# Kernel tuning notes

Measured on AMD Instinct MI355X. Metric: run time of the kernel, lower is better.

## Reference

```python
import jax, jax.numpy as jnp
import numpy as np

N = 50000   # nodes
E = 600000  # edges
F = 128     # feat_in
H = 64      # hidden_features
H2 = 32     # hidden_features // 2


def setup_inputs() -> dict:
    key = jax.random.key(0)
    ks = jax.random.split(key, 10)
    w = lambda k, shape: jax.random.normal(k, shape, dtype=jnp.float32) * 0.05
    return {
        "x": jax.random.normal(ks[0], (N, F), dtype=jnp.float32),
        "edge_index": jax.random.randint(ks[1], (2, E), 0, N, dtype=jnp.int32),
        "edge_attr": jax.random.uniform(ks[2], (E, 1), dtype=jnp.float32),
        # GINConv 1 MLP: Linear(F,H) -> Linear(H,H), learnable eps
        "w1a": w(ks[3], (H, F)), "b1a": jnp.zeros((H,), jnp.float32),
        "w1b": w(ks[4], (H, H)), "b1b": jnp.zeros((H,), jnp.float32),
        "eps1": jnp.zeros((), jnp.float32),
        # GINConv 2 MLP: Linear(H,H2) -> Linear(H2,H2), learnable eps
        "w2a": w(ks[5], (H2, H)), "b2a": jnp.zeros((H2,), jnp.float32),
        "w2b": w(ks[6], (H2, H2)), "b2b": jnp.zeros((H2,), jnp.float32),
        "eps2": jnp.zeros((), jnp.float32),
        # SAGEConv(H2, 1): lin_l (neighbor path, has bias), lin_r (root path, no bias)
        "wl": w(ks[7], (1, H2)), "bl": jnp.zeros((1,), jnp.float32),
        "wr": w(ks[8], (1, H2)),
    }


def _gin(x, src, dst, eps, wa, ba, wb, bb):
    # GIN: MLP((1+eps)*x_i + sum_{j->i} x_j)
    agg = jax.ops.segment_sum(x[src], dst, num_segments=x.shape[0])
    h = (1.0 + eps) * x + agg
    h = h @ wa.T + ba
    return h @ wb.T + bb


def reference(x, edge_index, edge_attr, w1a, b1a, w1b, b1b, eps1,
              w2a, b2a, w2b, b2b, eps2, wl, bl, wr):
    src, dst = edge_index[0], edge_index[1]
    ew = edge_attr.squeeze()  # (E,)
    n = x.shape[0]

    h = jax.nn.relu(_gin(x, src, dst, eps1, w1a, b1a, w1b, b1b))
    # dropout is identity in eval mode
    h = jax.nn.relu(_gin(h, src, dst, eps2, w2a, b2a, w2b, b2b))

    # SAGEConv with edge weights: mean over weighted messages + root transform
    msg = ew[:, None] * h[src]                                   # (E, H2)
    num = jax.ops.segment_sum(msg, dst, num_segments=n)          # (N, H2)
    cnt = jax.ops.segment_sum(jnp.ones((msg.shape[0],), h.dtype), dst, num_segments=n)
    mean = num / jnp.maximum(cnt, 1.0)[:, None]
    out = mean @ wl.T + bl + h @ wr.T                            # (N, 1)
    return jax.nn.relu(out)
```

## Files before the change

### kernel.cpp

```cpp
#include <hip/hip_runtime.h>

#define N_NODES 50000
#define N_EDGES 600000
#define F_IN 128
#define H1 64
#define H2 32
#define NBLK ((N_NODES + 255) / 256)
#define PREP_BLOCKS 41
#define CNT_BLOCKS ((N_EDGES / 4 + 255) / 256)
#define GEMM1_BLOCKS ((N_NODES + 63) / 64)
#define FILL_BLOCKS ((N_EDGES / 4 + 255) / 256)

__device__ inline unsigned bf_round(float x) {
  unsigned u = __float_as_uint(x);
  u += 0x7FFFu + ((u >> 16) & 1u);
  return u >> 16;
}
__device__ inline unsigned pack_bf2(float a, float b) {
  return (bf_round(b) << 16) | bf_round(a);
}
__device__ inline float2 unpack_bf2(unsigned u) {
  return make_float2(__uint_as_float(u << 16), __uint_as_float(u & 0xFFFF0000u));
}

__global__ __launch_bounds__(256) void prep_and_count(
    const float* __restrict__ w1a, const float* __restrict__ b1a,
    const float* __restrict__ w1b, const float* __restrict__ b1b,
    const float* __restrict__ w2a, const float* __restrict__ b2a,
    const float* __restrict__ w2b, const float* __restrict__ b2b,
    float* __restrict__ M1, float* __restrict__ c1,
    float* __restrict__ M2, float* __restrict__ c2,
    const int* __restrict__ ei, int* __restrict__ counts) {
  if (blockIdx.x >= PREP_BLOCKS) {
    int t = (blockIdx.x - PREP_BLOCKS) * 256 + threadIdx.x;
    if (t < N_EDGES / 4) {
      int4 d4 = *reinterpret_cast<const int4*>(&ei[N_EDGES + t * 4]);
      atomicAdd(&counts[d4.x], 1);
      atomicAdd(&counts[d4.y], 1);
      atomicAdd(&counts[d4.z], 1);
      atomicAdd(&counts[d4.w], 1);
    }
    return;
  }
  int i = blockIdx.x * 256 + threadIdx.x;
  if (i < F_IN * H1) {
    int f = i >> 6, h = i & 63;
    float s = 0.f;
    for (int m = 0; m < H1; ++m) s += w1a[m * F_IN + f] * w1b[h * H1 + m];
    M1[i] = s;
    return;
  }
  i -= F_IN * H1;
  if (i < H1) {
    float s = b1b[i];
    for (int m = 0; m < H1; ++m) s += b1a[m] * w1b[i * H1 + m];
    c1[i] = s;
    return;
  }
  i -= H1;
  if (i < H1 * H2) {
    int h = i >> 5, o = i & 31;
    float s = 0.f;
    for (int m = 0; m < H2; ++m) s += w2a[m * H1 + h] * w2b[o * H2 + m];
    M2[i] = s;
    return;
  }
  i -= H1 * H2;
  if (i < H2) {
    float s = b2b[i];
    for (int m = 0; m < H2; ++m) s += b2a[m] * w2b[i * H2 + m];
    c2[i] = s;
  }
}

__global__ __launch_bounds__(256) void block_sums(const int* __restrict__ counts,
                                                  int* __restrict__ bsums) {
  __shared__ int s[256];
  int t = threadIdx.x;
  int i = blockIdx.x * 256 + t;
  s[t] = (i < N_NODES) ? counts[i] : 0;
  __syncthreads();
  for (int off = 128; off > 0; off >>= 1) {
    if (t < off) s[t] += s[t + off];
    __syncthreads();
  }
  if (t == 0) bsums[blockIdx.x] = s[0];
}

__global__ __launch_bounds__(256) void emit_rowptr(const int* __restrict__ counts,
                                                   const int* __restrict__ bsums,
                                                   int* __restrict__ row_ptr,
                                                   int* __restrict__ cursor) {
  __shared__ int sb[256];
  __shared__ int s[256];
  int t = threadIdx.x;
  int bv = (t < NBLK) ? bsums[t] : 0;
  sb[t] = bv;
  __syncthreads();
  for (int off = 1; off < 256; off <<= 1) {
    int u = (t >= off) ? sb[t - off] : 0;
    __syncthreads();
    sb[t] += u;
    __syncthreads();
  }
  if (blockIdx.x == 0 && t == NBLK - 1) row_ptr[N_NODES] = sb[t];
  int boff = (blockIdx.x == 0) ? 0 : sb[blockIdx.x - 1];
  int i = blockIdx.x * 256 + t;
  int v = (i < N_NODES) ? counts[i] : 0;
  s[t] = v;
  __syncthreads();
  for (int off = 1; off < 256; off <<= 1) {
    int u = (t >= off) ? s[t - off] : 0;
    __syncthreads();
    s[t] += u;
    __syncthreads();
  }
  if (i < N_NODES) {
    int ex = boff + s[t] - v;
    row_ptr[i] = ex;
    cursor[i] = ex;
  }
}

__global__ __launch_bounds__(256) void gemm1_fill(
    const float* __restrict__ x, const float* __restrict__ M1,
    unsigned* __restrict__ ybf, const int* __restrict__ ei,
    const float* __restrict__ ea, int* __restrict__ cursor,
    int2* __restrict__ csr) {
  __shared__ float sW[F_IN * H1];
  __shared__ float sX[32][H1];
  if (blockIdx.x >= GEMM1_BLOCKS) {
    int t = (blockIdx.x - GEMM1_BLOCKS) * 256 + threadIdx.x;
    if (t < N_EDGES / 4) {
      int4 s4 = *reinterpret_cast<const int4*>(&ei[4 * t]);
      int4 d4 = *reinterpret_cast<const int4*>(&ei[N_EDGES + 4 * t]);
      float4 w4 = *reinterpret_cast<const float4*>(&ea[4 * t]);
      int p0 = atomicAdd(&cursor[d4.x], 1);
      csr[p0] = make_int2(s4.x, __float_as_int(w4.x));
      int p1 = atomicAdd(&cursor[d4.y], 1);
      csr[p1] = make_int2(s4.y, __float_as_int(w4.y));
      int p2 = atomicAdd(&cursor[d4.z], 1);
      csr[p2] = make_int2(s4.z, __float_as_int(w4.z));
      int p3 = atomicAdd(&cursor[d4.w], 1);
      csr[p3] = make_int2(s4.w, __float_as_int(w4.w));
    }
    return;
  }
  int tid = threadIdx.x;
  for (int i = tid; i < F_IN * H1; i += 256) sW[i] = M1[i];

  int row0 = blockIdx.x * 64;
  int tr = tid >> 4;
  int tc = tid & 15;
  int lrow = tid & 63;
  int kgrp = tid >> 6;
  const float* xrow = x + (long long)(row0 + lrow) * F_IN;
  bool rvalid = (row0 + lrow) < N_NODES;

  float acc[4][4] = {{0.f}};

  for (int kc = 0; kc < 4; ++kc) {
    float4 v0 = make_float4(0.f, 0.f, 0.f, 0.f);
    float4 v1 = make_float4(0.f, 0.f, 0.f, 0.f);
    if (rvalid) {
      v0 = *reinterpret_cast<const float4*>(xrow + kc * 32 + kgrp * 8);
      v1 = *reinterpret_cast<const float4*>(xrow + kc * 32 + kgrp * 8 + 4);
    }
    __syncthreads();
    sX[kgrp * 8 + 0][lrow] = v0.x;
    sX[kgrp * 8 + 1][lrow] = v0.y;
    sX[kgrp * 8 + 2][lrow] = v0.z;
    sX[kgrp * 8 + 3][lrow] = v0.w;
    sX[kgrp * 8 + 4][lrow] = v1.x;
    sX[kgrp * 8 + 5][lrow] = v1.y;
    sX[kgrp * 8 + 6][lrow] = v1.z;
    sX[kgrp * 8 + 7][lrow] = v1.w;
    __syncthreads();
#pragma unroll
    for (int k = 0; k < 32; ++k) {
      float4 a = *reinterpret_cast<const float4*>(&sX[k][tr * 4]);
      float4 b = *reinterpret_cast<const float4*>(&sW[(kc * 32 + k) * H1 + tc * 4]);
      acc[0][0] += a.x * b.x; acc[0][1] += a.x * b.y;
      acc[0][2] += a.x * b.z; acc[0][3] += a.x * b.w;
      acc[1][0] += a.y * b.x; acc[1][1] += a.y * b.y;
      acc[1][2] += a.y * b.z; acc[1][3] += a.y * b.w;
      acc[2][0] += a.z * b.x; acc[2][1] += a.z * b.y;
      acc[2][2] += a.z * b.z; acc[2][3] += a.z * b.w;
      acc[3][0] += a.w * b.x; acc[3][1] += a.w * b.y;
      acc[3][2] += a.w * b.z; acc[3][3] += a.w * b.w;
    }
  }
#pragma unroll
  for (int i = 0; i < 4; ++i) {
    int row = row0 + tr * 4 + i;
    if (row < N_NODES) {
      uint2 o;
      o.x = pack_bf2(acc[i][0], acc[i][1]);
      o.y = pack_bf2(acc[i][2], acc[i][3]);
      *reinterpret_cast<uint2*>(&ybf[(unsigned)row * 32 + tc * 2]) = o;
    }
  }
}

__global__ __launch_bounds__(256) void agg_h(
    const unsigned* __restrict__ ybf, const int* __restrict__ row_ptr,
    const int2* __restrict__ csr, const float* __restrict__ c1,
    const float* __restrict__ eps1p, float* __restrict__ h) {
  int tid = threadIdx.x;
  int node = blockIdx.x * 4 + (tid >> 6);
  if (node >= N_NODES) return;
  int lane = tid & 63;
  int half = lane >> 5;
  int j = lane & 31;
  int start = row_ptr[node], end = row_ptr[node + 1];
  int mid = start + ((end - start + 1) >> 1);
  int b0 = half ? mid : start;
  int b1 = half ? end : mid;
  float a0 = 0.f, a1 = 0.f;
  int e = b0;
  for (; e + 4 <= b1; e += 4) {
    int s0 = csr[e + 0].x;
    int s1 = csr[e + 1].x;
    int s2 = csr[e + 2].x;
    int s3 = csr[e + 3].x;
    float2 u0 = unpack_bf2(ybf[(unsigned)s0 * 32 + j]);
    float2 u1 = unpack_bf2(ybf[(unsigned)s1 * 32 + j]);
    float2 u2 = unpack_bf2(ybf[(unsigned)s2 * 32 + j]);
    float2 u3 = unpack_bf2(ybf[(unsigned)s3 * 32 + j]);
    a0 += (u0.x + u1.x) + (u2.x + u3.x);
    a1 += (u0.y + u1.y) + (u2.y + u3.y);
  }
  float2 t0 = make_float2(0.f, 0.f), t1 = make_float2(0.f, 0.f),
         t2 = make_float2(0.f, 0.f);
  if (e + 0 < b1) t0 = unpack_bf2(ybf[(unsigned)csr[e + 0].x * 32 + j]);
  if (e + 1 < b1) t1 = unpack_bf2(ybf[(unsigned)csr[e + 1].x * 32 + j]);
  if (e + 2 < b1) t2 = unpack_bf2(ybf[(unsigned)csr[e + 2].x * 32 + j]);
  a0 += (t0.x + t1.x) + t2.x;
  a1 += (t0.y + t1.y) + t2.y;
  a0 += __shfl_xor(a0, 32);
  a1 += __shfl_xor(a1, 32);
  if (half == 0) {
    float eps1 = 1.0f + *eps1p;
    float2 self = unpack_bf2(ybf[(unsigned)node * 32 + j]);
    float2 c = *reinterpret_cast<const float2*>(&c1[2 * j]);
    float2 hv;
    hv.x = fmaxf(eps1 * self.x + a0 + c.x, 0.f);
    hv.y = fmaxf(eps1 * self.y + a1 + c.y, 0.f);
    *reinterpret_cast<float2*>(&h[(unsigned)node * H1 + 2 * j]) = hv;
  }
}

__global__ __launch_bounds__(256) void gemm2(const float* __restrict__ h,
                                             const float* __restrict__ M2,
                                             unsigned* __restrict__ zbf) {
  __shared__ float sW[H1 * H2];
  __shared__ float sX[H1][64];
  int tid = threadIdx.x;
  for (int i = tid; i < H1 * H2; i += 256) sW[i] = M2[i];

  int row0 = blockIdx.x * 64;
  int lrow = tid & 63;
  int kg = tid >> 6;
  bool rv = (row0 + lrow) < N_NODES;
  float4 v[4] = {};
  if (rv) {
    const float* hr = h + (long long)(row0 + lrow) * H1 + kg * 16;
#pragma unroll
    for (int q = 0; q < 4; ++q) v[q] = *reinterpret_cast<const float4*>(hr + q * 4);
  }
#pragma unroll
  for (int q = 0; q < 4; ++q) {
    sX[kg * 16 + q * 4 + 0][lrow] = v[q].x;
    sX[kg * 16 + q * 4 + 1][lrow] = v[q].y;
    sX[kg * 16 + q * 4 + 2][lrow] = v[q].z;
    sX[kg * 16 + q * 4 + 3][lrow] = v[q].w;
  }
  __syncthreads();
  int tr = tid >> 4;
  int tc = tid & 15;
  float acc[4][2] = {{0.f}};
#pragma unroll
  for (int k = 0; k < H1; ++k) {
    float4 a = *reinterpret_cast<const float4*>(&sX[k][tr * 4]);
    float2 b = *reinterpret_cast<const float2*>(&sW[k * H2 + tc * 2]);
    acc[0][0] += a.x * b.x; acc[0][1] += a.x * b.y;
    acc[1][0] += a.y * b.x; acc[1][1] += a.y * b.y;
    acc[2][0] += a.z * b.x; acc[2][1] += a.z * b.y;
    acc[3][0] += a.w * b.x; acc[3][1] += a.w * b.y;
  }
#pragma unroll
  for (int i = 0; i < 4; ++i) {
    int row = row0 + tr * 4 + i;
    if (row < N_NODES)
      zbf[(unsigned)row * 16 + tc] = pack_bf2(acc[i][0], acc[i][1]);
  }
}

__global__ __launch_bounds__(256) void gin3(
    const unsigned* __restrict__ zbf, const int* __restrict__ row_ptr,
    const int2* __restrict__ csr, const float* __restrict__ c2,
    const float* __restrict__ eps2p, const float* __restrict__ wl,
    const float* __restrict__ wr, float* __restrict__ p,
    float* __restrict__ r) {
  int tid = blockIdx.x * 256 + threadIdx.x;
  int node = tid >> 4;
  if (node >= N_NODES) return;
  int j = tid & 15;
  int start = row_ptr[node], end = row_ptr[node + 1];
  float a0 = 0.f, a1 = 0.f;
  int e = start;
  for (; e + 8 <= end; e += 8) {
    int s0 = csr[e + 0].x; int s1 = csr[e + 1].x;
    int s2 = csr[e + 2].x; int s3 = csr[e + 3].x;
    int s4 = csr[e + 4].x; int s5 = csr[e + 5].x;
    int s6 = csr[e + 6].x; int s7 = csr[e + 7].x;
    float2 u0 = unpack_bf2(zbf[(unsigned)s0 * 16 + j]);
    float2 u1 = unpack_bf2(zbf[(unsigned)s1 * 16 + j]);
    float2 u2 = unpack_bf2(zbf[(unsigned)s2 * 16 + j]);
    float2 u3 = unpack_bf2(zbf[(unsigned)s3 * 16 + j]);
    float2 u4 = unpack_bf2(zbf[(unsigned)s4 * 16 + j]);
    float2 u5 = unpack_bf2(zbf[(unsigned)s5 * 16 + j]);
    float2 u6 = unpack_bf2(zbf[(unsigned)s6 * 16 + j]);
    float2 u7 = unpack_bf2(zbf[(unsigned)s7 * 16 + j]);
    a0 += ((u0.x + u1.x) + (u2.x + u3.x)) + ((u4.x + u5.x) + (u6.x + u7.x));
    a1 += ((u0.y + u1.y) + (u2.y + u3.y)) + ((u4.y + u5.y) + (u6.y + u7.y));
  }
  for (; e + 4 <= end; e += 4) {
    int s0 = csr[e + 0].x; int s1 = csr[e + 1].x;
    int s2 = csr[e + 2].x; int s3 = csr[e + 3].x;
    float2 u0 = unpack_bf2(zbf[(unsigned)s0 * 16 + j]);
    float2 u1 = unpack_bf2(zbf[(unsigned)s1 * 16 + j]);
    float2 u2 = unpack_bf2(zbf[(unsigned)s2 * 16 + j]);
    float2 u3 = unpack_bf2(zbf[(unsigned)s3 * 16 + j]);
    a0 += (u0.x + u1.x) + (u2.x + u3.x);
    a1 += (u0.y + u1.y) + (u2.y + u3.y);
  }
  float2 t0 = make_float2(0.f, 0.f), t1 = make_float2(0.f, 0.f),
         t2 = make_float2(0.f, 0.f);
  if (e + 0 < end) t0 = unpack_bf2(zbf[(unsigned)csr[e + 0].x * 16 + j]);
  if (e + 1 < end) t1 = unpack_bf2(zbf[(unsigned)csr[e + 1].x * 16 + j]);
  if (e + 2 < end) t2 = unpack_bf2(zbf[(unsigned)csr[e + 2].x * 16 + j]);
  a0 += (t0.x + t1.x) + t2.x;
  a1 += (t0.y + t1.y) + t2.y;
  float eps2 = 1.0f + *eps2p;
  float2 self = unpack_bf2(zbf[(unsigned)node * 16 + j]);
  float2 c = *reinterpret_cast<const float2*>(&c2[2 * j]);
  float h0 = fmaxf(eps2 * self.x + a0 + c.x, 0.f);
  float h1 = fmaxf(eps2 * self.y + a1 + c.y, 0.f);
  float2 l = *reinterpret_cast<const float2*>(&wl[2 * j]);
  float2 w = *reinterpret_cast<const float2*>(&wr[2 * j]);
  float pd = h0 * l.x + h1 * l.y;
  float rd = h0 * w.x + h1 * w.y;
#pragma unroll
  for (int m = 8; m >= 1; m >>= 1) {
    pd += __shfl_xor(pd, m, 16);
    rd += __shfl_xor(rd, m, 16);
  }
  if (j == 0) {
    p[node] = pd;
    r[node] = rd;
  }
}

__global__ __launch_bounds__(256) void sage_out(
    const int* __restrict__ row_ptr, const int2* __restrict__ csr,
    const float* __restrict__ p, const float* __restrict__ r,
    const float* __restrict__ blp, float* __restrict__ out) {
  int idx = blockIdx.x * 256 + threadIdx.x;
  int node = idx >> 4;
  if (node >= N_NODES) return;
  int l = idx & 15;
  int start = row_ptr[node], end = row_ptr[node + 1];
  float acc = 0.f;
  for (int e = start + l; e < end; e += 16) {
    int2 c = csr[e];
    acc += __int_as_float(c.y) * p[c.x];
  }
#pragma unroll
  for (int m = 8; m >= 1; m >>= 1) acc += __shfl_xor(acc, m, 16);
  if (l == 0) {
    float mean = acc / fmaxf((float)(end - start), 1.0f);
    out[node] = fmaxf(mean + blp[0] + r[node], 0.f);
  }
}

extern "C" void kernel_launch(void* const* d_in, const int* in_sizes, int n_in,
                              void* d_out, int out_size, void* d_ws,
                              size_t ws_size, hipStream_t stream) {
  const float* x = (const float*)d_in[0];
  const int* ei = (const int*)d_in[1];
  const float* ea = (const float*)d_in[2];
  const float* w1a = (const float*)d_in[3];
  const float* b1a = (const float*)d_in[4];
  const float* w1b = (const float*)d_in[5];
  const float* b1b = (const float*)d_in[6];
  const float* eps1 = (const float*)d_in[7];
  const float* w2a = (const float*)d_in[8];
  const float* b2a = (const float*)d_in[9];
  const float* w2b = (const float*)d_in[10];
  const float* b2b = (const float*)d_in[11];
  const float* eps2 = (const float*)d_in[12];
  const float* wl = (const float*)d_in[13];
  const float* bl = (const float*)d_in[14];
  const float* wr = (const float*)d_in[15];
  float* out = (float*)d_out;

  float* ws = (float*)d_ws;
  float* M1 = ws;
  float* c1 = M1 + F_IN * H1;
  float* M2 = c1 + H1;
  float* c2 = M2 + H1 * H2;
  unsigned* ybf = (unsigned*)(c2 + H2);
  float* h = (float*)(ybf + (size_t)N_NODES * 32);
  unsigned* zbf = (unsigned*)(h + (size_t)N_NODES * H1);
  float* p = (float*)(zbf + (size_t)N_NODES * 16);
  float* r = p + N_NODES;
  int2* csr = (int2*)(r + N_NODES);
  int* counts = (int*)(csr + N_EDGES);
  int* cursor = counts + N_NODES;
  int* bsums = cursor + N_NODES;
  int* row_ptr = bsums + NBLK;

  hipMemsetAsync(counts, 0, sizeof(int) * (size_t)N_NODES, stream);

  prep_and_count<<<PREP_BLOCKS + CNT_BLOCKS, 256, 0, stream>>>(
      w1a, b1a, w1b, b1b, w2a, b2a, w2b, b2b, M1, c1, M2, c2, ei, counts);

  block_sums<<<NBLK, 256, 0, stream>>>(counts, bsums);
  emit_rowptr<<<NBLK, 256, 0, stream>>>(counts, bsums, row_ptr, cursor);

  gemm1_fill<<<GEMM1_BLOCKS + FILL_BLOCKS, 256, 0, stream>>>(
      x, M1, ybf, ei, ea, cursor, csr);

  agg_h<<<(N_NODES + 3) / 4, 256, 0, stream>>>(ybf, row_ptr, csr, c1, eps1, h);

  gemm2<<<(N_NODES + 63) / 64, 256, 0, stream>>>(h, M2, zbf);

  gin3<<<(N_NODES * 16 + 255) / 256, 256, 0, stream>>>(zbf, row_ptr, csr, c2,
                                                       eps2, wl, wr, p, r);

  sage_out<<<(N_NODES * 16 + 255) / 256, 256, 0, stream>>>(row_ptr, csr, p, r,
                                                           bl, out);
}
```

Measured before the change: 223.0 us.

## Replace two-pass scan with atomic segment allocation and widen gather loads

Merges the block-sum and row-pointer scan kernels into one kernel that reserves each block's CSR range with an atomicAdd on a global counter. Segments are no longer in node order, so each node's end now comes from the cursor left by the fill pass instead of row_ptr[node+1]. The two gather kernels are also reorganized: each lane loads 8 bytes (four bf16 values) and several edges are gathered in parallel within a wavefront, then reduced with shuffles. The change removes one launch and one scan pass and aims for more memory parallelism in the gathers, at the cost of a non-deterministic CSR ordering and extra shuffle reductions.

```diff
diff --git a/kernel.cpp b/kernel.cpp
--- a/kernel.cpp
+++ b/kernel.cpp
@@ -73,38 +73,12 @@
   }
 }
 
-__global__ __launch_bounds__(256) void block_sums(const int* __restrict__ counts,
-                                                  int* __restrict__ bsums) {
+__global__ __launch_bounds__(256) void assign_segments(
+    const int* __restrict__ counts, int* __restrict__ total,
+    int* __restrict__ row_ptr, int* __restrict__ cursor) {
   __shared__ int s[256];
+  __shared__ int base;
   int t = threadIdx.x;
-  int i = blockIdx.x * 256 + t;
-  s[t] = (i < N_NODES) ? counts[i] : 0;
-  __syncthreads();
-  for (int off = 128; off > 0; off >>= 1) {
-    if (t < off) s[t] += s[t + off];
-    __syncthreads();
-  }
-  if (t == 0) bsums[blockIdx.x] = s[0];
-}
-
-__global__ __launch_bounds__(256) void emit_rowptr(const int* __restrict__ counts,
-                                                   const int* __restrict__ bsums,
-                                                   int* __restrict__ row_ptr,
-                                                   int* __restrict__ cursor) {
-  __shared__ int sb[256];
-  __shared__ int s[256];
-  int t = threadIdx.x;
-  int bv = (t < NBLK) ? bsums[t] : 0;
-  sb[t] = bv;
-  __syncthreads();
-  for (int off = 1; off < 256; off <<= 1) {
-    int u = (t >= off) ? sb[t - off] : 0;
-    __syncthreads();
-    sb[t] += u;
-    __syncthreads();
-  }
-  if (blockIdx.x == 0 && t == NBLK - 1) row_ptr[N_NODES] = sb[t];
-  int boff = (blockIdx.x == 0) ? 0 : sb[blockIdx.x - 1];
   int i = blockIdx.x * 256 + t;
   int v = (i < N_NODES) ? counts[i] : 0;
   s[t] = v;
@@ -115,8 +89,10 @@
     s[t] += u;
     __syncthreads();
   }
+  if (t == 255) base = atomicAdd(total, s[255]);
+  __syncthreads();
   if (i < N_NODES) {
-    int ex = boff + s[t] - v;
+    int ex = base + s[t] - v;
     row_ptr[i] = ex;
     cursor[i] = ex;
   }
@@ -204,49 +180,56 @@
 
 __global__ __launch_bounds__(256) void agg_h(
     const unsigned* __restrict__ ybf, const int* __restrict__ row_ptr,
-    const int2* __restrict__ csr, const float* __restrict__ c1,
-    const float* __restrict__ eps1p, float* __restrict__ h) {
+    const int* __restrict__ row_end, const int2* __restrict__ csr,
+    const float* __restrict__ c1, const float* __restrict__ eps1p,
+    float* __restrict__ h) {
   int tid = threadIdx.x;
   int node = blockIdx.x * 4 + (tid >> 6);
   if (node >= N_NODES) return;
   int lane = tid & 63;
-  int half = lane >> 5;
-  int j = lane & 31;
-  int start = row_ptr[node], end = row_ptr[node + 1];
-  int mid = start + ((end - start + 1) >> 1);
-  int b0 = half ? mid : start;
-  int b1 = half ? end : mid;
-  float a0 = 0.f, a1 = 0.f;
-  int e = b0;
-  for (; e + 4 <= b1; e += 4) {
-    int s0 = csr[e + 0].x;
-    int s1 = csr[e + 1].x;
-    int s2 = csr[e + 2].x;
-    int s3 = csr[e + 3].x;
-    float2 u0 = unpack_bf2(ybf[(unsigned)s0 * 32 + j]);
-    float2 u1 = unpack_bf2(ybf[(unsigned)s1 * 32 + j]);
-    float2 u2 = unpack_bf2(ybf[(unsigned)s2 * 32 + j]);
-    float2 u3 = unpack_bf2(ybf[(unsigned)s3 * 32 + j]);
-    a0 += (u0.x + u1.x) + (u2.x + u3.x);
-    a1 += (u0.y + u1.y) + (u2.y + u3.y);
-  }
-  float2 t0 = make_float2(0.f, 0.f), t1 = make_float2(0.f, 0.f),
-         t2 = make_float2(0.f, 0.f);
-  if (e + 0 < b1) t0 = unpack_bf2(ybf[(unsigned)csr[e + 0].x * 32 + j]);
-  if (e + 1 < b1) t1 = unpack_bf2(ybf[(unsigned)csr[e + 1].x * 32 + j]);
-  if (e + 2 < b1) t2 = unpack_bf2(ybf[(unsigned)csr[e + 2].x * 32 + j]);
-  a0 += (t0.x + t1.x) + t2.x;
-  a1 += (t0.y + t1.y) + t2.y;
-  a0 += __shfl_xor(a0, 32);
-  a1 += __shfl_xor(a1, 32);
-  if (half == 0) {
+  int g = lane >> 4;
+  int q = lane & 15;
+  int start = row_ptr[node], end = row_end[node];
+  float a0 = 0.f, a1 = 0.f, a2 = 0.f, a3 = 0.f;
+  for (int e0 = start; e0 < end; e0 += 16) {
+    int e_0 = e0 + g;
+    int e_1 = e0 + 4 + g;
+    int e_2 = e0 + 8 + g;
+    int e_3 = e0 + 12 + g;
+    uint2 v0 = make_uint2(0u, 0u), v1 = make_uint2(0u, 0u),
+          v2 = make_uint2(0u, 0u), v3 = make_uint2(0u, 0u);
+    if (e_0 < end)
+      v0 = *reinterpret_cast<const uint2*>(&ybf[(unsigned)csr[e_0].x * 32 + q * 2]);
+    if (e_1 < end)
+      v1 = *reinterpret_cast<const uint2*>(&ybf[(unsigned)csr[e_1].x * 32 + q * 2]);
+    if (e_2 < end)
+      v2 = *reinterpret_cast<const uint2*>(&ybf[(unsigned)csr[e_2].x * 32 + q * 2]);
+    if (e_3 < end)
+      v3 = *reinterpret_cast<const uint2*>(&ybf[(unsigned)csr[e_3].x * 32 + q * 2]);
+    float2 u00 = unpack_bf2(v0.x), u01 = unpack_bf2(v0.y);
+    float2 u10 = unpack_bf2(v1.x), u11 = unpack_bf2(v1.y);
+    float2 u20 = unpack_bf2(v2.x), u21 = unpack_bf2(v2.y);
+    float2 u30 = unpack_bf2(v3.x), u31 = unpack_bf2(v3.y);
+    a0 += (u00.x + u10.x) + (u20.x + u30.x);
+    a1 += (u00.y + u10.y) + (u20.y + u30.y);
+    a2 += (u01.x + u11.x) + (u21.x + u31.x);
+    a3 += (u01.y + u11.y) + (u21.y + u31.y);
+  }
+  a0 += __shfl_xor(a0, 16); a0 += __shfl_xor(a0, 32);
+  a1 += __shfl_xor(a1, 16); a1 += __shfl_xor(a1, 32);
+  a2 += __shfl_xor(a2, 16); a2 += __shfl_xor(a2, 32);
+  a3 += __shfl_xor(a3, 16); a3 += __shfl_xor(a3, 32);
+  if (g == 0) {
     float eps1 = 1.0f + *eps1p;
-    float2 self = unpack_bf2(ybf[(unsigned)node * 32 + j]);
-    float2 c = *reinterpret_cast<const float2*>(&c1[2 * j]);
-    float2 hv;
-    hv.x = fmaxf(eps1 * self.x + a0 + c.x, 0.f);
-    hv.y = fmaxf(eps1 * self.y + a1 + c.y, 0.f);
-    *reinterpret_cast<float2*>(&h[(unsigned)node * H1 + 2 * j]) = hv;
+    uint2 sv = *reinterpret_cast<const uint2*>(&ybf[(unsigned)node * 32 + q * 2]);
+    float2 s0 = unpack_bf2(sv.x), s1 = unpack_bf2(sv.y);
+    float4 c = *reinterpret_cast<const float4*>(&c1[4 * q]);
+    float4 hv;
+    hv.x = fmaxf(eps1 * s0.x + a0 + c.x, 0.f);
+    hv.y = fmaxf(eps1 * s0.y + a1 + c.y, 0.f);
+    hv.z = fmaxf(eps1 * s1.x + a2 + c.z, 0.f);
+    hv.w = fmaxf(eps1 * s1.y + a3 + c.w, 0.f);
+    *reinterpret_cast<float4*>(&h[(unsigned)node * H1 + 4 * q]) = hv;
   }
 }
 
@@ -298,79 +281,78 @@
 
 __global__ __launch_bounds__(256) void gin3(
     const unsigned* __restrict__ zbf, const int* __restrict__ row_ptr,
-    const int2* __restrict__ csr, const float* __restrict__ c2,
-    const float* __restrict__ eps2p, const float* __restrict__ wl,
-    const float* __restrict__ wr, float* __restrict__ p,
-    float* __restrict__ r) {
-  int tid = blockIdx.x * 256 + threadIdx.x;
-  int node = tid >> 4;
+    const int* __restrict__ row_end, const int2* __restrict__ csr,
+    const float* __restrict__ c2, const float* __restrict__ eps2p,
+    const float* __restrict__ wl, const float* __restrict__ wr,
+    float* __restrict__ p, float* __restrict__ r) {
+  int idx = blockIdx.x * 256 + threadIdx.x;
+  int node = idx >> 5;
   if (node >= N_NODES) return;
-  int j = tid & 15;
-  int start = row_ptr[node], end = row_ptr[node + 1];
-  float a0 = 0.f, a1 = 0.f;
-  int e = start;
-  for (; e + 8 <= end; e += 8) {
-    int s0 = csr[e + 0].x; int s1 = csr[e + 1].x;
-    int s2 = csr[e + 2].x; int s3 = csr[e + 3].x;
-    int s4 = csr[e + 4].x; int s5 = csr[e + 5].x;
-    int s6 = csr[e + 6].x; int s7 = csr[e + 7].x;
-    float2 u0 = unpack_bf2(zbf[(unsigned)s0 * 16 + j]);
-    float2 u1 = unpack_bf2(zbf[(unsigned)s1 * 16 + j]);
-    float2 u2 = unpack_bf2(zbf[(unsigned)s2 * 16 + j]);
-    float2 u3 = unpack_bf2(zbf[(unsigned)s3 * 16 + j]);
-    float2 u4 = unpack_bf2(zbf[(unsigned)s4 * 16 + j]);
-    float2 u5 = unpack_bf2(zbf[(unsigned)s5 * 16 + j]);
-    float2 u6 = unpack_bf2(zbf[(unsigned)s6 * 16 + j]);
-    float2 u7 = unpack_bf2(zbf[(unsigned)s7 * 16 + j]);
-    a0 += ((u0.x + u1.x) + (u2.x + u3.x)) + ((u4.x + u5.x) + (u6.x + u7.x));
-    a1 += ((u0.y + u1.y) + (u2.y + u3.y)) + ((u4.y + u5.y) + (u6.y + u7.y));
-  }
-  for (; e + 4 <= end; e += 4) {
-    int s0 = csr[e + 0].x; int s1 = csr[e + 1].x;
-    int s2 = csr[e + 2].x; int s3 = csr[e + 3].x;
-    float2 u0 = unpack_bf2(zbf[(unsigned)s0 * 16 + j]);
-    float2 u1 = unpack_bf2(zbf[(unsigned)s1 * 16 + j]);
-    float2 u2 = unpack_bf2(zbf[(unsigned)s2 * 16 + j]);
-    float2 u3 = unpack_bf2(zbf[(unsigned)s3 * 16 + j]);
-    a0 += (u0.x + u1.x) + (u2.x + u3.x);
-    a1 += (u0.y + u1.y) + (u2.y + u3.y);
-  }
-  float2 t0 = make_float2(0.f, 0.f), t1 = make_float2(0.f, 0.f),
-         t2 = make_float2(0.f, 0.f);
-  if (e + 0 < end) t0 = unpack_bf2(zbf[(unsigned)csr[e + 0].x * 16 + j]);
-  if (e + 1 < end) t1 = unpack_bf2(zbf[(unsigned)csr[e + 1].x * 16 + j]);
-  if (e + 2 < end) t2 = unpack_bf2(zbf[(unsigned)csr[e + 2].x * 16 + j]);
-  a0 += (t0.x + t1.x) + t2.x;
-  a1 += (t0.y + t1.y) + t2.y;
-  float eps2 = 1.0f + *eps2p;
-  float2 self = unpack_bf2(zbf[(unsigned)node * 16 + j]);
-  float2 c = *reinterpret_cast<const float2*>(&c2[2 * j]);
-  float h0 = fmaxf(eps2 * self.x + a0 + c.x, 0.f);
-  float h1 = fmaxf(eps2 * self.y + a1 + c.y, 0.f);
-  float2 l = *reinterpret_cast<const float2*>(&wl[2 * j]);
-  float2 w = *reinterpret_cast<const float2*>(&wr[2 * j]);
-  float pd = h0 * l.x + h1 * l.y;
-  float rd = h0 * w.x + h1 * w.y;
-#pragma unroll
-  for (int m = 8; m >= 1; m >>= 1) {
-    pd += __shfl_xor(pd, m, 16);
-    rd += __shfl_xor(rd, m, 16);
-  }
-  if (j == 0) {
-    p[node] = pd;
-    r[node] = rd;
+  int l = idx & 31;
+  int g = l >> 3;
+  int q = l & 7;
+  int start = row_ptr[node], end = row_end[node];
+  float a0 = 0.f, a1 = 0.f, a2 = 0.f, a3 = 0.f;
+  for (int e0 = start; e0 < end; e0 += 16) {
+    int e_0 = e0 + g;
+    int e_1 = e0 + 4 + g;
+    int e_2 = e0 + 8 + g;
+    int e_3 = e0 + 12 + g;
+    uint2 v0 = make_uint2(0u, 0u), v1 = make_uint2(0u, 0u),
+          v2 = make_uint2(0u, 0u), v3 = make_uint2(0u, 0u);
+    if (e_0 < end)
+      v0 = *reinterpret_cast<const uint2*>(&zbf[(unsigned)csr[e_0].x * 16 + q * 2]);
+    if (e_1 < end)
+      v1 = *reinterpret_cast<const uint2*>(&zbf[(unsigned)csr[e_1].x * 16 + q * 2]);
+    if (e_2 < end)
+      v2 = *reinterpret_cast<const uint2*>(&zbf[(unsigned)csr[e_2].x * 16 + q * 2]);
+    if (e_3 < end)
+      v3 = *reinterpret_cast<const uint2*>(&zbf[(unsigned)csr[e_3].x * 16 + q * 2]);
+    float2 u00 = unpack_bf2(v0.x), u01 = unpack_bf2(v0.y);
+    float2 u10 = unpack_bf2(v1.x), u11 = unpack_bf2(v1.y);
+    float2 u20 = unpack_bf2(v2.x), u21 = unpack_bf2(v2.y);
+    float2 u30 = unpack_bf2(v3.x), u31 = unpack_bf2(v3.y);
+    a0 += (u00.x + u10.x) + (u20.x + u30.x);
+    a1 += (u00.y + u10.y) + (u20.y + u30.y);
+    a2 += (u01.x + u11.x) + (u21.x + u31.x);
+    a3 += (u01.y + u11.y) + (u21.y + u31.y);
+  }
+  a0 += __shfl_xor(a0, 8, 32); a0 += __shfl_xor(a0, 16, 32);
+  a1 += __shfl_xor(a1, 8, 32); a1 += __shfl_xor(a1, 16, 32);
+  a2 += __shfl_xor(a2, 8, 32); a2 += __shfl_xor(a2, 16, 32);
+  a3 += __shfl_xor(a3, 8, 32); a3 += __shfl_xor(a3, 16, 32);
+  if (g == 0) {
+    float eps2 = 1.0f + *eps2p;
+    uint2 sv = *reinterpret_cast<const uint2*>(&zbf[(unsigned)node * 16 + q * 2]);
+    float2 s0 = unpack_bf2(sv.x), s1 = unpack_bf2(sv.y);
+    float4 c = *reinterpret_cast<const float4*>(&c2[4 * q]);
+    float h0 = fmaxf(eps2 * s0.x + a0 + c.x, 0.f);
+    float h1 = fmaxf(eps2 * s0.y + a1 + c.y, 0.f);
+    float h2 = fmaxf(eps2 * s1.x + a2 + c.z, 0.f);
+    float h3 = fmaxf(eps2 * s1.y + a3 + c.w, 0.f);
+    float4 wlv = *reinterpret_cast<const float4*>(&wl[4 * q]);
+    float4 wrv = *reinterpret_cast<const float4*>(&wr[4 * q]);
+    float pd = h0 * wlv.x + h1 * wlv.y + h2 * wlv.z + h3 * wlv.w;
+    float rd = h0 * wrv.x + h1 * wrv.y + h2 * wrv.z + h3 * wrv.w;
+    pd += __shfl_xor(pd, 4, 8); pd += __shfl_xor(pd, 2, 8); pd += __shfl_xor(pd, 1, 8);
+    rd += __shfl_xor(rd, 4, 8); rd += __shfl_xor(rd, 2, 8); rd += __shfl_xor(rd, 1, 8);
+    if (q == 0) {
+      p[node] = pd;
+      r[node] = rd;
+    }
   }
 }
 
 __global__ __launch_bounds__(256) void sage_out(
-    const int* __restrict__ row_ptr, const int2* __restrict__ csr,
-    const float* __restrict__ p, const float* __restrict__ r,
-    const float* __restrict__ blp, float* __restrict__ out) {
+    const int* __restrict__ row_ptr, const int* __restrict__ row_end,
+    const int2* __restrict__ csr, const float* __restrict__ p,
+    const float* __restrict__ r, const float* __restrict__ blp,
+    float* __restrict__ out) {
   int idx = blockIdx.x * 256 + threadIdx.x;
   int node = idx >> 4;
   if (node >= N_NODES) return;
   int l = idx & 15;
-  int start = row_ptr[node], end = row_ptr[node + 1];
+  int start = row_ptr[node], end = row_end[node];
   float acc = 0.f;
   for (int e = start + l; e < end; e += 16) {
     int2 c = csr[e];
@@ -417,28 +399,28 @@
   float* r = p + N_NODES;
   int2* csr = (int2*)(r + N_NODES);
   int* counts = (int*)(csr + N_EDGES);
-  int* cursor = counts + N_NODES;
-  int* bsums = cursor + N_NODES;
-  int* row_ptr = bsums + NBLK;
-
-  hipMemsetAsync(counts, 0, sizeof(int) * (size_t)N_NODES, stream);
+  int* total = counts + N_NODES;
+  int* cursor = total + 1;
+  int* row_ptr = cursor + N_NODES;
+
+  hipMemsetAsync(counts, 0, sizeof(int) * (size_t)(N_NODES + 1), stream);
 
   prep_and_count<<<PREP_BLOCKS + CNT_BLOCKS, 256, 0, stream>>>(
       w1a, b1a, w1b, b1b, w2a, b2a, w2b, b2b, M1, c1, M2, c2, ei, counts);
 
-  block_sums<<<NBLK, 256, 0, stream>>>(counts, bsums);
-  emit_rowptr<<<NBLK, 256, 0, stream>>>(counts, bsums, row_ptr, cursor);
+  assign_segments<<<NBLK, 256, 0, stream>>>(counts, total, row_ptr, cursor);
 
   gemm1_fill<<<GEMM1_BLOCKS + FILL_BLOCKS, 256, 0, stream>>>(
       x, M1, ybf, ei, ea, cursor, csr);
 
-  agg_h<<<(N_NODES + 3) / 4, 256, 0, stream>>>(ybf, row_ptr, csr, c1, eps1, h);
+  agg_h<<<(N_NODES + 3) / 4, 256, 0, stream>>>(ybf, row_ptr, cursor, csr, c1,
+                                               eps1, h);
 
   gemm2<<<(N_NODES + 63) / 64, 256, 0, stream>>>(h, M2, zbf);
 
-  gin3<<<(N_NODES * 16 + 255) / 256, 256, 0, stream>>>(zbf, row_ptr, csr, c2,
-                                                       eps2, wl, wr, p, r);
-
-  sage_out<<<(N_NODES * 16 + 255) / 256, 256, 0, stream>>>(row_ptr, csr, p, r,
-                                                           bl, out);
-}
+  gin3<<<(N_NODES * 32 + 255) / 256, 256, 0, stream>>>(
+      zbf, row_ptr, cursor, csr, c2, eps2, wl, wr, p, r);
+
+  sage_out<<<(N_NODES * 16 + 255) / 256, 256, 0, stream>>>(row_ptr, cursor,
+                                                           csr, p, r, bl, out);
+}
```

Measured after the change: 223.4 us. No clear change (+0.2%).
